# Performance work log

Hardware: AMD Instinct MI355X
Metric: run time of the kernel (lower is better)

The kernel has to match this reference:

```python
import jax, jax.numpy as jnp
import numpy as np

B, S, D = 4, 4096, 2048
DECAY_BIAS_INIT = -4.0
W_SCALE = 0.02


def setup_inputs() -> dict:
    key = jax.random.key(0)
    ks = jax.random.split(key, 6)
    return {
        "x": jax.random.normal(ks[0], (B, S, D), dtype=jnp.float32),
        "W_in": jax.random.normal(ks[1], (D, D), dtype=jnp.float32) * W_SCALE,
        "b_in": jnp.zeros((D,), jnp.float32),
        "W_decay": jax.random.normal(ks[2], (D, D), dtype=jnp.float32) * W_SCALE,
        "b_decay": jnp.zeros((D,), jnp.float32),
        "W_gate": jax.random.normal(ks[3], (D, D), dtype=jnp.float32) * W_SCALE,
        "b_gate": jnp.zeros((D,), jnp.float32),
        "W_out": jax.random.normal(ks[4], (D, D), dtype=jnp.float32) * W_SCALE,
        "b_out": jnp.zeros((D,), jnp.float32),
        "decay_bias": jnp.full((D,), DECAY_BIAS_INIT, jnp.float32),
    }


def reference(x, W_in, b_in, W_decay, b_decay, W_gate, b_gate, W_out, b_out, decay_bias):
    # Projections (weights stored as [in, out]; torch Linear applies x @ W.T, here W is pre-transposed)
    inp = jax.nn.silu(jnp.einsum("bsd,de->bse", x, W_in) + b_in).astype(jnp.float32)
    decay = jax.nn.sigmoid(jnp.einsum("bsd,de->bse", x, W_decay) + b_decay + decay_bias)
    gate = jax.nn.sigmoid(jnp.einsum("bsd,de->bse", x, W_gate) + b_gate)

    # Gated linear recurrence: s_t = d_t * s_{t-1} + (1 - d_t) * i_t
    def step(state, di):
        d, i = di
        state = d * state + (1.0 - d) * i
        return state, state

    init = jnp.zeros((x.shape[0], x.shape[2]), jnp.float32)
    _, states = jax.lax.scan(
        step, init, (jnp.swapaxes(decay, 0, 1), jnp.swapaxes(inp, 0, 1))
    )  # states: [S, B, D]
    y = gate * jnp.swapaxes(states, 0, 1)  # [B, S, D]
    y = y.astype(x.dtype)
    return jnp.einsum("bsd,de->bse", y, W_out) + b_out
```

## Files before the change

kernel.cpp:

```cpp
#include <hip/hip_runtime.h>

typedef unsigned short u16;
typedef __attribute__((ext_vector_type(4))) float f4;
typedef __attribute__((ext_vector_type(8))) short s8v;
typedef __attribute__((ext_vector_type(8))) unsigned short u16x8;
typedef __attribute__((ext_vector_type(4))) unsigned short u16x4;

#define B_   4
#define S_   4096
#define D_   2048
#define M_   (B_ * S_)
#define K_   D_
#define N3_  (3 * D_)
#define CCH  128
#define LCH  32
#define NTK  32

__device__ __forceinline__ u16 f2bf(float f) {
  unsigned u = __float_as_uint(f);
  u += 0x7FFF + ((u >> 16) & 1);
  return (u16)(u >> 16);
}
__device__ __forceinline__ float bf2f(u16 h) {
  return __uint_as_float(((unsigned)h) << 16);
}
__device__ __forceinline__ float sigm(float z) {
  return 1.0f / (1.0f + __expf(-z));
}

__global__ void k_cvt(const float* __restrict__ src, u16* __restrict__ dst, int n4) {
  int i = blockIdx.x * 256 + threadIdx.x;
  if (i >= n4) return;
  f4 v = *(const f4*)(src + (size_t)i * 4);
  u16x4 o;
  o[0] = f2bf(v[0]); o[1] = f2bf(v[1]); o[2] = f2bf(v[2]); o[3] = f2bf(v[3]);
  *(u16x4*)(dst + (size_t)i * 4) = o;
}

__global__ void k_tcvt(const float* __restrict__ src, u16* __restrict__ dst) {
  __shared__ float tile[32][33];
  int tx = threadIdx.x & 31, ty = threadIdx.x >> 5;
  int c0 = blockIdx.x * 32, r0 = blockIdx.y * 32;
#pragma unroll
  for (int j = 0; j < 32; j += 8)
    tile[ty + j][tx] = src[(size_t)(r0 + ty + j) * 2048 + c0 + tx];
  __syncthreads();
#pragma unroll
  for (int j = 0; j < 32; j += 8)
    dst[(size_t)(c0 + ty + j) * 2048 + r0 + tx] = f2bf(tile[tx][ty + j]);
}

__global__ void __launch_bounds__(512, 2)
k_gemm256(const u16* __restrict__ A, const u16* __restrict__ BT, int N, int mode,
          u16* __restrict__ o_inp, u16* __restrict__ o_dec, u16* __restrict__ o_gate,
          const float* __restrict__ b_in, const float* __restrict__ b_dec,
          const float* __restrict__ b_gate, const float* __restrict__ dbias,
          float* __restrict__ o_f, const float* __restrict__ b_out) {
  extern __shared__ u16 smem[];
  u16* const Asb[2] = { smem,         smem + 16384 };
  u16* const Bsb[2] = { smem + 32768, smem + 49152 };

  const int ntn = N >> 8;
  const int nwg = gridDim.x;
  const int bid = blockIdx.x;
  const int wg = (bid & 7) * (nwg >> 3) + (bid >> 3);
  const int tile_m = (wg / ntn) << 8;
  const int tile_n = (wg % ntn) << 8;
  const int tid = threadIdx.x;
  const int wave = tid >> 6, lane = tid & 63;
  const int wm = (wave >> 2) << 7;
  const int wn = (wave & 3) << 6;
  const int l15 = lane & 15, lhi = lane >> 4;
  const int srow = tid >> 3, sslot = tid & 7;

  f4 acc[8][4];
#pragma unroll
  for (int m = 0; m < 8; ++m)
#pragma unroll
    for (int n = 0; n < 4; ++n)
#pragma unroll
      for (int r = 0; r < 4; ++r) acc[m][n][r] = 0.0f;

  s8v afr2[2][2][2];
  s8v bfr[2][4];

  auto STAGE = [&](const u16* __restrict__ G, int grow0, u16* L, int c, int k0) {
    int r = (c << 6) + srow;
    int sc = (sslot ^ (r & 7)) << 3;
    __builtin_amdgcn_global_load_lds(
        (const __attribute__((address_space(1))) unsigned int*)(G + (size_t)(grow0 + r) * K_ + k0 + sc),
        (__attribute__((address_space(3))) unsigned int*)(L + (((c << 6) + (wave << 3)) << 6)),
        16, 0, 0);
  };

#pragma unroll
  for (int c = 0; c < 4; ++c) STAGE(A, tile_m, Asb[0], c, 0);
#pragma unroll
  for (int c = 0; c < 4; ++c) STAGE(BT, tile_n, Bsb[0], c, 0);
#pragma unroll
  for (int c = 0; c < 4; ++c) STAGE(BT, tile_n, Bsb[1], c, 64);
  STAGE(A, tile_m, Asb[1], 0, 64);
  STAGE(A, tile_m, Asb[1], 2, 64);
  asm volatile("s_waitcnt vmcnt(6)" ::: "memory");
  __builtin_amdgcn_s_barrier();

#pragma unroll
  for (int kk = 0; kk < 2; ++kk)
#pragma unroll
    for (int mi = 0; mi < 2; ++mi) {
      int r = wm + (mi << 4) + l15;
      afr2[0][mi][kk] = *(const s8v*)(Asb[0] + (r << 6) + ((((kk << 2) + lhi) ^ (r & 7)) << 3));
    }
#pragma unroll
  for (int kk = 0; kk < 2; ++kk)
#pragma unroll
    for (int n = 0; n < 4; ++n) {
      int r = wn + (n << 4) + l15;
      bfr[kk][n] = *(const s8v*)(Bsb[0] + (r << 6) + ((((kk << 2) + lhi) ^ (r & 7)) << 3));
    }

#pragma unroll 1
  for (int it = 0; it < NTK / 2; ++it) {
    const int t0 = it << 1;
#pragma unroll
    for (int p = 0; p < 8; ++p) {
      const int toff[8] = {1, 2, 2, 2, 2, 3, 3, 3};
      const int sopA[8] = {1, 0, 0, 1, 1, 0, 0, 1};
      const int sc0[8]  = {1, 0, 2, 0, 1, 0, 2, 0};
      const int sc1f[8] = {3, 1, 3, 2, 3, 1, 3, 2};
      const int q = p & 3;

      {
        const int st = (t0 + toff[p]) & (NTK - 1);
        const int k0s = st << 6;
        u16* const Ad = Asb[st & 1];
        u16* const Bd = Bsb[st & 1];
        if (sopA[p]) { STAGE(A, tile_m, Ad, sc0[p], k0s); STAGE(A, tile_m, Ad, sc1f[p], k0s); }
        else         { STAGE(BT, tile_n, Bd, sc0[p], k0s); STAGE(BT, tile_n, Bd, sc1f[p], k0s); }
      }
      if (q == 3) {
        asm volatile("s_waitcnt vmcnt(6)" ::: "memory");
        __builtin_amdgcn_sched_barrier(0);
      }
      __builtin_amdgcn_s_barrier();

      {
        const int pn = p + 1;
        const int qn = pn & 3, bn = (pn >> 2) & 1, as = pn & 1;
        u16* const Anx = Asb[bn];
#pragma unroll
        for (int kk = 0; kk < 2; ++kk)
#pragma unroll
          for (int mi = 0; mi < 2; ++mi) {
            int r = wm + ((qn * 2 + mi) << 4) + l15;
            afr2[as][mi][kk] = *(const s8v*)(Anx + (r << 6) + ((((kk << 2) + lhi) ^ (r & 7)) << 3));
          }
      }

      __builtin_amdgcn_s_setprio(1);
#pragma unroll
      for (int kk = 0; kk < 2; ++kk)
#pragma unroll
        for (int mi = 0; mi < 2; ++mi)
#pragma unroll
          for (int n = 0; n < 4; ++n)
            acc[q * 2 + mi][n] =
                __builtin_amdgcn_mfma_f32_16x16x32_bf16(afr2[p & 1][mi][kk], bfr[kk][n],
                                                        acc[q * 2 + mi][n], 0, 0, 0);
      __builtin_amdgcn_s_setprio(0);

      if (q == 3) {
        const int bn = ((p + 1) >> 2) & 1;
        u16* const Bnx = Bsb[bn];
#pragma unroll
        for (int kk = 0; kk < 2; ++kk)
#pragma unroll
          for (int n = 0; n < 4; ++n) {
            int r = wn + (n << 4) + l15;
            bfr[kk][n] = *(const s8v*)(Bnx + (r << 6) + ((((kk << 2) + lhi) ^ (r & 7)) << 3));
          }
      }
      __builtin_amdgcn_s_barrier();
    }
  }

  asm volatile("s_waitcnt vmcnt(0)" ::: "memory");
  __builtin_amdgcn_s_barrier();

  if (mode == 0) {
    const int selb = tile_n >> 11;
    const int dbase = tile_n & 2047;
    float bias[4];
#pragma unroll
    for (int n = 0; n < 4; ++n) {
      int d = dbase + wn + (n << 4) + l15;
      bias[n] = (selb == 0) ? b_in[d] : (selb == 1) ? (b_dec[d] + dbias[d]) : b_gate[d];
    }
#pragma unroll
    for (int m = 0; m < 8; ++m)
#pragma unroll
      for (int n = 0; n < 4; ++n)
#pragma unroll
        for (int r = 0; r < 4; ++r) {
          int lrow = wm + (m << 4) + (lhi << 2) + r;
          int lcol = wn + (n << 4) + l15;
          float z = acc[m][n][r] + bias[n];
          float v = (selb == 0) ? z * sigm(z) : sigm(z);
          smem[(lrow << 8) + (((lcol >> 3) ^ (lrow & 7)) << 3) + (lcol & 7)] = f2bf(v);
        }
    __builtin_amdgcn_s_barrier();
    u16* const dst = (selb == 0) ? o_inp : (selb == 1) ? o_dec : o_gate;
    const int rr = tid >> 5, sl = tid & 31;
#pragma unroll
    for (int pass = 0; pass < 16; ++pass) {
      int row = (pass << 4) + rr;
      u16x8 v = *(const u16x8*)(smem + (row << 8) + ((sl ^ (row & 7)) << 3));
      *(u16x8*)(dst + (size_t)(tile_m + row) * D_ + dbase + (sl << 3)) = v;
    }
  } else {
    float* const Tf = (float*)smem;
    f4 bo = *(const f4*)(b_out + tile_n + (lane << 2));
#pragma unroll
    for (int sw = 0; sw < 2; ++sw) {
      if (sw) __builtin_amdgcn_s_barrier();
      if ((wm >> 7) == sw) {
#pragma unroll
        for (int m = 0; m < 8; ++m)
#pragma unroll
          for (int n = 0; n < 4; ++n)
#pragma unroll
            for (int r = 0; r < 4; ++r) {
              int lrow = (m << 4) + (lhi << 2) + r;
              int lcol = wn + (n << 4) + l15;
              Tf[(lrow << 8) + (((lcol >> 2) ^ (lrow & 7)) << 2) + (lcol & 3)] = acc[m][n][r];
            }
      }
      __builtin_amdgcn_s_barrier();
#pragma unroll
      for (int pass = 0; pass < 16; ++pass) {
        int lrow = (pass << 3) + wave;
        f4 v = *(const f4*)(Tf + (lrow << 8) + ((lane ^ (lrow & 7)) << 2));
        v[0] += bo[0]; v[1] += bo[1]; v[2] += bo[2]; v[3] += bo[3];
        *(f4*)(o_f + (size_t)(tile_m + (sw << 7) + lrow) * D_ + tile_n + (lane << 2)) = v;
      }
    }
  }
}

__global__ void k_scan1(const u16* __restrict__ dec, const u16* __restrict__ inp,
                        float* __restrict__ chA, float* __restrict__ chB) {
  int b = blockIdx.x / CCH, c = blockIdx.x % CCH;
  int d0 = threadIdx.x * 8;
  const u16* dp = dec + ((size_t)b * S_ + c * LCH) * D_ + d0;
  const u16* ip = inp + ((size_t)b * S_ + c * LCH) * D_ + d0;
  float Aa[8], st[8];
#pragma unroll
  for (int i = 0; i < 8; ++i) { Aa[i] = 1.0f; st[i] = 0.0f; }
#pragma unroll 4
  for (int j = 0; j < LCH; ++j) {
    u16x8 dv = *(const u16x8*)(dp + (size_t)j * D_);
    u16x8 iv = *(const u16x8*)(ip + (size_t)j * D_);
#pragma unroll
    for (int i = 0; i < 8; ++i) {
      float dd = bf2f(dv[i]), ii = bf2f(iv[i]);
      Aa[i] *= dd;
      st[i] = dd * st[i] + (1.0f - dd) * ii;
    }
  }
  size_t o = ((size_t)b * CCH + c) * D_ + d0;
#pragma unroll
  for (int i = 0; i < 8; ++i) { chA[o + i] = Aa[i]; chB[o + i] = st[i]; }
}

__global__ void k_scan2(const float* __restrict__ chA, const float* __restrict__ chB,
                        float* __restrict__ ini) {
  int b = blockIdx.x >> 3;
  int d = ((blockIdx.x & 7) << 8) + threadIdx.x;
  float st = 0.0f;
  for (int c = 0; c < CCH; ++c) {
    size_t o = ((size_t)b * CCH + c) * D_ + d;
    ini[o] = st;
    st = chA[o] * st + chB[o];
  }
}

__global__ void k_scan3(const u16* __restrict__ dec, const u16* __restrict__ inp,
                        const u16* __restrict__ gat, const float* __restrict__ ini,
                        u16* __restrict__ y) {
  int b = blockIdx.x / CCH, c = blockIdx.x % CCH;
  int d0 = threadIdx.x * 8;
  size_t ib = ((size_t)b * CCH + c) * D_ + d0;
  float st[8];
#pragma unroll
  for (int i = 0; i < 8; ++i) st[i] = ini[ib + i];
  size_t base = ((size_t)b * S_ + c * LCH) * D_ + d0;
#pragma unroll 4
  for (int j = 0; j < LCH; ++j) {
    size_t o = base + (size_t)j * D_;
    u16x8 dv = *(const u16x8*)(dec + o);
    u16x8 iv = *(const u16x8*)(inp + o);
    u16x8 gv = *(const u16x8*)(gat + o);
    u16x8 yv;
#pragma unroll
    for (int i = 0; i < 8; ++i) {
      float dd = bf2f(dv[i]), ii = bf2f(iv[i]);
      st[i] = dd * st[i] + (1.0f - dd) * ii;
      yv[i] = f2bf(bf2f(gv[i]) * st[i]);
    }
    *(u16x8*)(y + o) = yv;
  }
}

extern "C" void kernel_launch(void* const* d_in, const int* in_sizes, int n_in,
                              void* d_out, int out_size, void* d_ws, size_t ws_size,
                              hipStream_t stream) {
  (void)in_sizes; (void)n_in; (void)out_size; (void)ws_size;
  const float* x      = (const float*)d_in[0];
  const float* W_in   = (const float*)d_in[1];
  const float* b_in   = (const float*)d_in[2];
  const float* W_dec  = (const float*)d_in[3];
  const float* b_dec  = (const float*)d_in[4];
  const float* W_gate = (const float*)d_in[5];
  const float* b_gate = (const float*)d_in[6];
  const float* W_out  = (const float*)d_in[7];
  const float* b_out  = (const float*)d_in[8];
  const float* dbias  = (const float*)d_in[9];
  float* out = (float*)d_out;

  char* ws = (char*)d_ws;
  u16*   xb  = (u16*)(ws);
  u16*   w3t = (u16*)(ws + 67108864ull);
  u16*   wot = (u16*)(ws + 92274688ull);
  u16*   inp = (u16*)(ws + 100663296ull);
  u16*   dec = (u16*)(ws + 167772160ull);
  u16*   gat = (u16*)(ws + 234881024ull);
  float* chA = (float*)(ws + 301989888ull);
  float* chB = (float*)(ws + 306184192ull);
  float* ini = (float*)(ws + 310378496ull);
  u16*   y   = xb;

  hipFuncSetAttribute((const void*)k_gemm256,
                      hipFuncAttributeMaxDynamicSharedMemorySize, 131072);

  k_cvt<<<32768, 256, 0, stream>>>(x, xb, 8388608);
  k_tcvt<<<dim3(64, 64), 256, 0, stream>>>(W_in,   w3t);
  k_tcvt<<<dim3(64, 64), 256, 0, stream>>>(W_dec,  w3t + 2048 * 2048);
  k_tcvt<<<dim3(64, 64), 256, 0, stream>>>(W_gate, w3t + 2 * 2048 * 2048);
  k_tcvt<<<dim3(64, 64), 256, 0, stream>>>(W_out,  wot);

  k_gemm256<<<(M_ / 256) * (N3_ / 256), 512, 131072, stream>>>(
      xb, w3t, N3_, 0, inp, dec, gat, b_in, b_dec, b_gate, dbias, nullptr, nullptr);

  k_scan1<<<B_ * CCH, 256, 0, stream>>>(dec, inp, chA, chB);
  k_scan2<<<32, 256, 0, stream>>>(chA, chB, ini);
  k_scan3<<<B_ * CCH, 256, 0, stream>>>(dec, inp, gat, ini, y);

  k_gemm256<<<(M_ / 256) * (D_ / 256), 512, 131072, stream>>>(
      y, wot, D_, 1, nullptr, nullptr, nullptr, nullptr, nullptr, nullptr, nullptr,
      out, b_out);
}
```

Baseline: 665.0 us.

## Make GEMM persistent with cross-tile prefetch and spare-LDS epilogue

Turns the GEMM into a persistent kernel: 256 workgroups each process several consecutive tiles (6 for the fused projection, 2 for the output GEMM). On the last K iteration of a tile, the next tile's first K slices are prefetched into the double buffers. The epilogue goes through a separate 32 KB spare LDS region in smaller row slabs so it does not overwrite those prefetched buffers. This targets tail effects, per-block launch and prologue cost, and the pipeline drain between tiles, at the price of more LDS (160 KB), which may limit occupancy, more barriers in the epilogue, and the loss of the previous grouped tile ordering that helped L2 reuse.

```diff
diff --git a/kernel.cpp b/kernel.cpp
--- a/kernel.cpp
+++ b/kernel.cpp
@@ -52,6 +52,7 @@
 
 __global__ void __launch_bounds__(512, 2)
 k_gemm256(const u16* __restrict__ A, const u16* __restrict__ BT, int N, int mode,
+          int tpb,
           u16* __restrict__ o_inp, u16* __restrict__ o_dec, u16* __restrict__ o_gate,
           const float* __restrict__ b_in, const float* __restrict__ b_dec,
           const float* __restrict__ b_gate, const float* __restrict__ dbias,
@@ -59,13 +60,10 @@
   extern __shared__ u16 smem[];
   u16* const Asb[2] = { smem,         smem + 16384 };
   u16* const Bsb[2] = { smem + 32768, smem + 49152 };
+  u16* const spare  = smem + 65536;
 
   const int ntn = N >> 8;
-  const int nwg = gridDim.x;
-  const int bid = blockIdx.x;
-  const int wg = (bid & 7) * (nwg >> 3) + (bid >> 3);
-  const int tile_m = (wg / ntn) << 8;
-  const int tile_n = (wg % ntn) << 8;
+  const int g0 = blockIdx.x * tpb;
   const int tid = threadIdx.x;
   const int wave = tid >> 6, lane = tid & 63;
   const int wm = (wave >> 2) << 7;
@@ -93,157 +91,192 @@
         16, 0, 0);
   };
 
-#pragma unroll
-  for (int c = 0; c < 4; ++c) STAGE(A, tile_m, Asb[0], c, 0);
-#pragma unroll
-  for (int c = 0; c < 4; ++c) STAGE(BT, tile_n, Bsb[0], c, 0);
-#pragma unroll
-  for (int c = 0; c < 4; ++c) STAGE(BT, tile_n, Bsb[1], c, 64);
-  STAGE(A, tile_m, Asb[1], 0, 64);
-  STAGE(A, tile_m, Asb[1], 2, 64);
-  asm volatile("s_waitcnt vmcnt(6)" ::: "memory");
-  __builtin_amdgcn_s_barrier();
-
-#pragma unroll
-  for (int kk = 0; kk < 2; ++kk)
-#pragma unroll
-    for (int mi = 0; mi < 2; ++mi) {
-      int r = wm + (mi << 4) + l15;
-      afr2[0][mi][kk] = *(const s8v*)(Asb[0] + (r << 6) + ((((kk << 2) + lhi) ^ (r & 7)) << 3));
+  {
+    const int tm0 = (g0 / ntn) << 8, tn0 = (g0 % ntn) << 8;
+#pragma unroll
+    for (int c = 0; c < 4; ++c) STAGE(A, tm0, Asb[0], c, 0);
+#pragma unroll
+    for (int c = 0; c < 4; ++c) STAGE(BT, tn0, Bsb[0], c, 0);
+#pragma unroll
+    for (int c = 0; c < 4; ++c) STAGE(BT, tn0, Bsb[1], c, 64);
+    STAGE(A, tm0, Asb[1], 0, 64);
+    STAGE(A, tm0, Asb[1], 2, 64);
+    asm volatile("s_waitcnt vmcnt(6)" ::: "memory");
+    __builtin_amdgcn_s_barrier();
+#pragma unroll
+    for (int kk = 0; kk < 2; ++kk)
+#pragma unroll
+      for (int mi = 0; mi < 2; ++mi) {
+        int r = wm + (mi << 4) + l15;
+        afr2[0][mi][kk] = *(const s8v*)(Asb[0] + (r << 6) + ((((kk << 2) + lhi) ^ (r & 7)) << 3));
+      }
+#pragma unroll
+    for (int kk = 0; kk < 2; ++kk)
+#pragma unroll
+      for (int n = 0; n < 4; ++n) {
+        int r = wn + (n << 4) + l15;
+        bfr[kk][n] = *(const s8v*)(Bsb[0] + (r << 6) + ((((kk << 2) + lhi) ^ (r & 7)) << 3));
+      }
+  }
+
+#pragma unroll 1
+  for (int t = 0; t < tpb; ++t) {
+    const int g = g0 + t;
+    const int tile_m = (g / ntn) << 8, tile_n = (g % ntn) << 8;
+    const int gn = (t + 1 < tpb) ? g + 1 : g;
+    const int tm_nx = (gn / ntn) << 8, tn_nx = (gn % ntn) << 8;
+
+#pragma unroll 1
+    for (int it = 0; it < NTK / 2; ++it) {
+      const int t0 = it << 1;
+      const int last_it = (it == NTK / 2 - 1);
+#pragma unroll
+      for (int p = 0; p < 8; ++p) {
+        const int toff[8] = {1, 2, 2, 2, 2, 3, 3, 3};
+        const int sopA[8] = {1, 0, 0, 1, 1, 0, 0, 1};
+        const int sc0[8]  = {1, 0, 2, 0, 1, 0, 2, 0};
+        const int sc1f[8] = {3, 1, 3, 2, 3, 1, 3, 2};
+        const int q = p & 3;
+
+        {
+          const int st = (t0 + toff[p]) & (NTK - 1);
+          const int k0s = st << 6;
+          const int nxt = last_it && p >= 1;
+          u16* const Ad = Asb[st & 1];
+          u16* const Bd = Bsb[st & 1];
+          if (sopA[p]) {
+            const int gm = nxt ? tm_nx : tile_m;
+            STAGE(A, gm, Ad, sc0[p], k0s); STAGE(A, gm, Ad, sc1f[p], k0s);
+          } else {
+            const int gb = nxt ? tn_nx : tile_n;
+            STAGE(BT, gb, Bd, sc0[p], k0s); STAGE(BT, gb, Bd, sc1f[p], k0s);
+          }
+        }
+        if (q == 3) {
+          asm volatile("s_waitcnt vmcnt(6)" ::: "memory");
+          __builtin_amdgcn_sched_barrier(0);
+        }
+        __builtin_amdgcn_s_barrier();
+
+        {
+          const int pn = p + 1;
+          const int qn = pn & 3, bn = (pn >> 2) & 1, as = pn & 1;
+          u16* const Anx = Asb[bn];
+#pragma unroll
+          for (int kk = 0; kk < 2; ++kk)
+#pragma unroll
+            for (int mi = 0; mi < 2; ++mi) {
+              int r = wm + ((qn * 2 + mi) << 4) + l15;
+              afr2[as][mi][kk] = *(const s8v*)(Anx + (r << 6) + ((((kk << 2) + lhi) ^ (r & 7)) << 3));
+            }
+        }
+
+        __builtin_amdgcn_s_setprio(1);
+#pragma unroll
+        for (int kk = 0; kk < 2; ++kk)
+#pragma unroll
+          for (int mi = 0; mi < 2; ++mi)
+#pragma unroll
+            for (int n = 0; n < 4; ++n)
+              acc[q * 2 + mi][n] =
+                  __builtin_amdgcn_mfma_f32_16x16x32_bf16(afr2[p & 1][mi][kk], bfr[kk][n],
+                                                          acc[q * 2 + mi][n], 0, 0, 0);
+        __builtin_amdgcn_s_setprio(0);
+
+        if (q == 3) {
+          const int bn = ((p + 1) >> 2) & 1;
+          u16* const Bnx = Bsb[bn];
+#pragma unroll
+          for (int kk = 0; kk < 2; ++kk)
+#pragma unroll
+            for (int n = 0; n < 4; ++n) {
+              int r = wn + (n << 4) + l15;
+              bfr[kk][n] = *(const s8v*)(Bnx + (r << 6) + ((((kk << 2) + lhi) ^ (r & 7)) << 3));
+            }
+        }
+        __builtin_amdgcn_s_barrier();
+      }
     }
-#pragma unroll
-  for (int kk = 0; kk < 2; ++kk)
-#pragma unroll
-    for (int n = 0; n < 4; ++n) {
-      int r = wn + (n << 4) + l15;
-      bfr[kk][n] = *(const s8v*)(Bsb[0] + (r << 6) + ((((kk << 2) + lhi) ^ (r & 7)) << 3));
+
+    if (mode == 0) {
+      const int selb = tile_n >> 11;
+      const int dbase = tile_n & 2047;
+      u16* const dst = (selb == 0) ? o_inp : (selb == 1) ? o_dec : o_gate;
+      float bias[4];
+#pragma unroll
+      for (int n = 0; n < 4; ++n) {
+        int d = dbase + wn + (n << 4) + l15;
+        bias[n] = (selb == 0) ? b_in[d] : (selb == 1) ? (b_dec[d] + dbias[d]) : b_gate[d];
+      }
+      const int rr = tid >> 5, sl = tid & 31;
+#pragma unroll
+      for (int sw = 0; sw < 4; ++sw) {
+        if ((wm >> 7) == (sw >> 1)) {
+          const int mb = (sw & 1) << 2;
+#pragma unroll
+          for (int mm = 0; mm < 4; ++mm) {
+#pragma unroll
+            for (int n = 0; n < 4; ++n)
+#pragma unroll
+              for (int r = 0; r < 4; ++r) {
+                int lr = (mm << 4) + (lhi << 2) + r;
+                int lcol = wn + (n << 4) + l15;
+                float z = acc[mb + mm][n][r] + bias[n];
+                float v = (selb == 0) ? z * sigm(z) : sigm(z);
+                spare[(lr << 8) + (((lcol >> 3) ^ (lr & 7)) << 3) + (lcol & 7)] = f2bf(v);
+              }
+          }
+        }
+        asm volatile("s_waitcnt lgkmcnt(0)" ::: "memory");
+        __builtin_amdgcn_s_barrier();
+#pragma unroll
+        for (int pass = 0; pass < 4; ++pass) {
+          int row = (pass << 4) + rr;
+          u16x8 v = *(const u16x8*)(spare + (row << 8) + ((sl ^ (row & 7)) << 3));
+          *(u16x8*)(dst + (size_t)(tile_m + (sw << 6) + row) * D_ + dbase + (sl << 3)) = v;
+        }
+        asm volatile("s_waitcnt lgkmcnt(0)" ::: "memory");
+        __builtin_amdgcn_s_barrier();
+      }
+    } else {
+      float* const Sf = (float*)spare;
+      f4 bo = *(const f4*)(b_out + tile_n + (lane << 2));
+#pragma unroll
+      for (int sw = 0; sw < 8; ++sw) {
+        if ((wm >> 7) == (sw >> 2)) {
+          const int mb = (sw & 3) << 1;
+#pragma unroll
+          for (int mm = 0; mm < 2; ++mm) {
+#pragma unroll
+            for (int n = 0; n < 4; ++n)
+#pragma unroll
+              for (int r = 0; r < 4; ++r) {
+                int lr = (mm << 4) + (lhi << 2) + r;
+                int lcol = wn + (n << 4) + l15;
+                Sf[(lr << 8) + (((lcol >> 2) ^ (lr & 7)) << 2) + (lcol & 3)] = acc[mb + mm][n][r];
+              }
+          }
+        }
+        asm volatile("s_waitcnt lgkmcnt(0)" ::: "memory");
+        __builtin_amdgcn_s_barrier();
+#pragma unroll
+        for (int pass = 0; pass < 4; ++pass) {
+          int row = (pass << 3) + wave;
+          f4 v = *(const f4*)(Sf + (row << 8) + ((lane ^ (row & 7)) << 2));
+          v[0] += bo[0]; v[1] += bo[1]; v[2] += bo[2]; v[3] += bo[3];
+          *(f4*)(o_f + (size_t)(tile_m + (sw << 5) + row) * D_ + tile_n + (lane << 2)) = v;
+        }
+        asm volatile("s_waitcnt lgkmcnt(0)" ::: "memory");
+        __builtin_amdgcn_s_barrier();
+      }
     }
 
-#pragma unroll 1
-  for (int it = 0; it < NTK / 2; ++it) {
-    const int t0 = it << 1;
-#pragma unroll
-    for (int p = 0; p < 8; ++p) {
-      const int toff[8] = {1, 2, 2, 2, 2, 3, 3, 3};
-      const int sopA[8] = {1, 0, 0, 1, 1, 0, 0, 1};
-      const int sc0[8]  = {1, 0, 2, 0, 1, 0, 2, 0};
-      const int sc1f[8] = {3, 1, 3, 2, 3, 1, 3, 2};
-      const int q = p & 3;
-
-      {
-        const int st = (t0 + toff[p]) & (NTK - 1);
-        const int k0s = st << 6;
-        u16* const Ad = Asb[st & 1];
-        u16* const Bd = Bsb[st & 1];
-        if (sopA[p]) { STAGE(A, tile_m, Ad, sc0[p], k0s); STAGE(A, tile_m, Ad, sc1f[p], k0s); }
-        else         { STAGE(BT, tile_n, Bd, sc0[p], k0s); STAGE(BT, tile_n, Bd, sc1f[p], k0s); }
-      }
-      if (q == 3) {
-        asm volatile("s_waitcnt vmcnt(6)" ::: "memory");
-        __builtin_amdgcn_sched_barrier(0);
-      }
-      __builtin_amdgcn_s_barrier();
-
-      {
-        const int pn = p + 1;
-        const int qn = pn & 3, bn = (pn >> 2) & 1, as = pn & 1;
-        u16* const Anx = Asb[bn];
-#pragma unroll
-        for (int kk = 0; kk < 2; ++kk)
-#pragma unroll
-          for (int mi = 0; mi < 2; ++mi) {
-            int r = wm + ((qn * 2 + mi) << 4) + l15;
-            afr2[as][mi][kk] = *(const s8v*)(Anx + (r << 6) + ((((kk << 2) + lhi) ^ (r & 7)) << 3));
-          }
-      }
-
-      __builtin_amdgcn_s_setprio(1);
-#pragma unroll
-      for (int kk = 0; kk < 2; ++kk)
-#pragma unroll
-        for (int mi = 0; mi < 2; ++mi)
-#pragma unroll
-          for (int n = 0; n < 4; ++n)
-            acc[q * 2 + mi][n] =
-                __builtin_amdgcn_mfma_f32_16x16x32_bf16(afr2[p & 1][mi][kk], bfr[kk][n],
-                                                        acc[q * 2 + mi][n], 0, 0, 0);
-      __builtin_amdgcn_s_setprio(0);
-
-      if (q == 3) {
-        const int bn = ((p + 1) >> 2) & 1;
-        u16* const Bnx = Bsb[bn];
-#pragma unroll
-        for (int kk = 0; kk < 2; ++kk)
-#pragma unroll
-          for (int n = 0; n < 4; ++n) {
-            int r = wn + (n << 4) + l15;
-            bfr[kk][n] = *(const s8v*)(Bnx + (r << 6) + ((((kk << 2) + lhi) ^ (r & 7)) << 3));
-          }
-      }
-      __builtin_amdgcn_s_barrier();
-    }
-  }
-
-  asm volatile("s_waitcnt vmcnt(0)" ::: "memory");
-  __builtin_amdgcn_s_barrier();
-
-  if (mode == 0) {
-    const int selb = tile_n >> 11;
-    const int dbase = tile_n & 2047;
-    float bias[4];
-#pragma unroll
-    for (int n = 0; n < 4; ++n) {
-      int d = dbase + wn + (n << 4) + l15;
-      bias[n] = (selb == 0) ? b_in[d] : (selb == 1) ? (b_dec[d] + dbias[d]) : b_gate[d];
-    }
 #pragma unroll
     for (int m = 0; m < 8; ++m)
 #pragma unroll
       for (int n = 0; n < 4; ++n)
 #pragma unroll
-        for (int r = 0; r < 4; ++r) {
-          int lrow = wm + (m << 4) + (lhi << 2) + r;
-          int lcol = wn + (n << 4) + l15;
-          float z = acc[m][n][r] + bias[n];
-          float v = (selb == 0) ? z * sigm(z) : sigm(z);
-          smem[(lrow << 8) + (((lcol >> 3) ^ (lrow & 7)) << 3) + (lcol & 7)] = f2bf(v);
-        }
-    __builtin_amdgcn_s_barrier();
-    u16* const dst = (selb == 0) ? o_inp : (selb == 1) ? o_dec : o_gate;
-    const int rr = tid >> 5, sl = tid & 31;
-#pragma unroll
-    for (int pass = 0; pass < 16; ++pass) {
-      int row = (pass << 4) + rr;
-      u16x8 v = *(const u16x8*)(smem + (row << 8) + ((sl ^ (row & 7)) << 3));
-      *(u16x8*)(dst + (size_t)(tile_m + row) * D_ + dbase + (sl << 3)) = v;
-    }
-  } else {
-    float* const Tf = (float*)smem;
-    f4 bo = *(const f4*)(b_out + tile_n + (lane << 2));
-#pragma unroll
-    for (int sw = 0; sw < 2; ++sw) {
-      if (sw) __builtin_amdgcn_s_barrier();
-      if ((wm >> 7) == sw) {
-#pragma unroll
-        for (int m = 0; m < 8; ++m)
-#pragma unroll
-          for (int n = 0; n < 4; ++n)
-#pragma unroll
-            for (int r = 0; r < 4; ++r) {
-              int lrow = (m << 4) + (lhi << 2) + r;
-              int lcol = wn + (n << 4) + l15;
-              Tf[(lrow << 8) + (((lcol >> 2) ^ (lrow & 7)) << 2) + (lcol & 3)] = acc[m][n][r];
-            }
-      }
-      __builtin_amdgcn_s_barrier();
-#pragma unroll
-      for (int pass = 0; pass < 16; ++pass) {
-        int lrow = (pass << 3) + wave;
-        f4 v = *(const f4*)(Tf + (lrow << 8) + ((lane ^ (lrow & 7)) << 2));
-        v[0] += bo[0]; v[1] += bo[1]; v[2] += bo[2]; v[3] += bo[3];
-        *(f4*)(o_f + (size_t)(tile_m + (sw << 7) + lrow) * D_ + tile_n + (lane << 2)) = v;
-      }
-    }
+        for (int r = 0; r < 4; ++r) acc[m][n][r] = 0.0f;
   }
 }
 
@@ -340,7 +373,7 @@
   u16*   y   = xb;
 
   hipFuncSetAttribute((const void*)k_gemm256,
-                      hipFuncAttributeMaxDynamicSharedMemorySize, 131072);
+                      hipFuncAttributeMaxDynamicSharedMemorySize, 163840);
 
   k_cvt<<<32768, 256, 0, stream>>>(x, xb, 8388608);
   k_tcvt<<<dim3(64, 64), 256, 0, stream>>>(W_in,   w3t);
@@ -348,14 +381,14 @@
   k_tcvt<<<dim3(64, 64), 256, 0, stream>>>(W_gate, w3t + 2 * 2048 * 2048);
   k_tcvt<<<dim3(64, 64), 256, 0, stream>>>(W_out,  wot);
 
-  k_gemm256<<<(M_ / 256) * (N3_ / 256), 512, 131072, stream>>>(
-      xb, w3t, N3_, 0, inp, dec, gat, b_in, b_dec, b_gate, dbias, nullptr, nullptr);
+  k_gemm256<<<256, 512, 163840, stream>>>(
+      xb, w3t, N3_, 0, 6, inp, dec, gat, b_in, b_dec, b_gate, dbias, nullptr, nullptr);
 
   k_scan1<<<B_ * CCH, 256, 0, stream>>>(dec, inp, chA, chB);
   k_scan2<<<32, 256, 0, stream>>>(chA, chB, ini);
   k_scan3<<<B_ * CCH, 256, 0, stream>>>(dec, inp, gat, ini, y);
 
-  k_gemm256<<<(M_ / 256) * (D_ / 256), 512, 131072, stream>>>(
-      y, wot, D_, 1, nullptr, nullptr, nullptr, nullptr, nullptr, nullptr, nullptr,
+  k_gemm256<<<256, 512, 163840, stream>>>(
+      y, wot, D_, 1, 2, nullptr, nullptr, nullptr, nullptr, nullptr, nullptr, nullptr,
       out, b_out);
 }
```

After: 946.6 us. +42.3%, slower.
